# Performance work log

Measured on AMD Instinct MI355X. Metric: run time of the kernel, lower is better.

## Reference

```python
import jax, jax.numpy as jnp
import numpy as np

B, IN, H, CTX = 16384, 1024, 1024, 2048


def setup_inputs() -> dict:
    key = jax.random.key(0)
    ks = jax.random.split(key, 20)
    stdv = 1.0 / np.sqrt(H)
    u = lambda k, shape: jax.random.uniform(k, shape, jnp.float32, -stdv, stdv)
    inp = {
        "y": jax.random.normal(ks[0], (B, IN), jnp.float32),
        "ctx": jax.random.normal(ks[1], (B, CTX), jnp.float32),
        "c0": jax.random.normal(ks[2], (B, H), jnp.float32),
        "h0": jax.random.normal(ks[3], (B, H), jnp.float32),
        # Concatenated gate weights in order (i, f, o, c), matching the
        # per-gate matrices Wi..Wc, Ui..Uc, Ci..Cc of the original module.
        "W": u(ks[4], (4 * H, IN)),   # input projections
        "U": u(ks[5], (4 * H, H)),    # hidden projections
        "C": u(ks[6], (4 * H, CTX)),  # context projections
        "b": u(ks[7], (4 * H,)),      # gate biases
    }
    return inp


def reference(y, ctx, c0, h0, W, U, C, b):
    # One fused GEMM per input stream instead of 12 small ones; same math.
    gates = y @ W.T + h0 @ U.T + ctx @ C.T + b  # [B, 4H]
    gi, gf, go, gc = jnp.split(gates, 4, axis=-1)
    i = jax.nn.sigmoid(gi)
    f = jax.nn.sigmoid(gf)
    o = jax.nn.sigmoid(go)
    c_hat = jnp.tanh(gc)
    c = i * c_hat + f * c0
    h = o * jnp.tanh(c)
    return (c, h)
```

## Files before the change

### kernel.cpp

```cpp
#include <hip/hip_runtime.h>
#include <hip/hip_bf16.h>
#include <stdint.h>

typedef __attribute__((ext_vector_type(8))) short short8;
typedef __attribute__((ext_vector_type(8))) unsigned short ushort8;
typedef __attribute__((ext_vector_type(4))) float f32x4;
typedef __attribute__((ext_vector_type(8))) __bf16 bf16x8;

#define GAS __attribute__((address_space(1)))
#define LAS __attribute__((address_space(3)))

static constexpr int Bn = 16384;
static constexpr int Hn = 1024;
static constexpr int KT = 4096;
static constexpr int BM = 256;
static constexpr int NT = KT / 64;

#define SBAR()   __builtin_amdgcn_s_barrier()
#define VMCNT(n) asm volatile("s_waitcnt vmcnt(" #n ")" ::: "memory")

__device__ __forceinline__ unsigned short f2bf(float f) {
  unsigned u = __builtin_bit_cast(unsigned, f);
  u = (u + 0x7FFFu + ((u >> 16) & 1u)) >> 16;
  return (unsigned short)u;
}

__device__ __forceinline__ float fast_sigm(float x) {
  return __builtin_amdgcn_rcpf(1.f + __expf(-x));
}
__device__ __forceinline__ float fast_tanh(float x) {
  return 1.f - 2.f * __builtin_amdgcn_rcpf(__expf(2.f * x) + 1.f);
}

__global__ __launch_bounds__(256) void cvt_concat_k(
    const float* __restrict__ s0, const float* __restrict__ s1,
    const float* __restrict__ s2, unsigned short* __restrict__ dst,
    long long n8) {
  long long stride = (long long)gridDim.x * blockDim.x;
  for (long long g = (long long)blockIdx.x * blockDim.x + threadIdx.x; g < n8;
       g += stride) {
    long long row = g >> 9;
    int cg = (int)(g & 511) << 3;
    const float* src;
    if (cg < 1024)      src = s0 + row * 1024 + cg;
    else if (cg < 2048) src = s1 + row * 1024 + (cg - 1024);
    else                src = s2 + row * 2048 + (cg - 2048);
    float4 f0 = *(const float4*)src;
    float4 f1 = *(const float4*)(src + 4);
    ushort8 o;
    o[0] = f2bf(f0.x); o[1] = f2bf(f0.y); o[2] = f2bf(f0.z); o[3] = f2bf(f0.w);
    o[4] = f2bf(f1.x); o[5] = f2bf(f1.y); o[6] = f2bf(f1.z); o[7] = f2bf(f1.w);
    *(ushort8*)(dst + (g << 3)) = o;
  }
}

__global__ __launch_bounds__(512, 2) void lstm_gemm(
    const unsigned short* __restrict__ X, const unsigned short* __restrict__ Wc,
    const float* __restrict__ bias, const float* __restrict__ c0,
    float* __restrict__ out_c, float* __restrict__ out_h) {
  extern __shared__ char smem[];

  int bid = blockIdx.x;
  int swz = (bid & 7) * 128 + (bid >> 3);
  int mblk = swz >> 4, cblk = swz & 15;
  int brow0 = mblk * BM;
  int hcol0 = cblk * 64;

  int tid = threadIdx.x;
  int lane = tid & 63, wid = tid >> 6;
  int wr = wid >> 2, wc = wid & 3;

  const char* Xc = (const char*)X;
  const char* Wcc = (const char*)Wc;

  int rr = tid >> 3;
  uint32_t cbyte = (uint32_t)(((tid & 7) * 16) ^ ((rr & 7) << 4));
  uint32_t aoff[2][2], boff[2][2];
#pragma unroll
  for (int half = 0; half < 2; ++half) {
#pragma unroll
    for (int j = 0; j < 2; ++j) {
      int r = half * 128 + j * 64 + rr;
      aoff[half][j] = (uint32_t)(brow0 + r) * (KT * 2) + cbyte;
      int w = ((r >> 4) & 3) * 1024 + hcol0 + ((r >> 6) << 4) + (r & 15);
      boff[half][j] = (uint32_t)w * (KT * 2) + cbyte;
    }
  }

  auto stage_half = [&](int isB, int half, int tt) {
    int ts = tt < NT ? tt : NT - 1;
    int bufs = tt & 1;
#pragma unroll
    for (int j = 0; j < 2; ++j) {
      uint32_t off = (isB ? boff[half][j] : aoff[half][j]) + (uint32_t)ts * 128u;
      const char* src = (isB ? Wcc : Xc) + off;
      char* dst = smem + bufs * 65536 + isB * 32768 + half * 16384 + j * 8192 +
                  wid * 1024;
      __builtin_amdgcn_global_load_lds((const GAS unsigned int*)src,
                                       (LAS unsigned int*)dst, 16, 0, 0);
    }
  };

  int kg = (lane >> 4) << 4;
  int sw = (lane & 7) << 4;
  int koff0 = (0 + kg) ^ sw;
  int koff1 = (64 + kg) ^ sw;
  int fr = lane & 15;

  f32x4 acc[8][4] = {};
  short8 bfr[4][2];

  stage_half(1, 0, 0);
  stage_half(1, 1, 0);
  stage_half(0, 0, 0);
  stage_half(0, 1, 0);
  stage_half(1, 0, 1);
  stage_half(1, 1, 1);
  stage_half(0, 0, 1);
  VMCNT(8);
  SBAR();

  for (int t = 0; t < NT; ++t) {
    int p = t & 1;
#pragma unroll
    for (int q = 0; q < 4; ++q) {
      if (q == 0) {
        int bb = p * 65536 + 32768 + (wc * 64 + fr) * 128;
#pragma unroll
        for (int n = 0; n < 4; ++n) {
          bfr[n][0] = *(const short8*)(smem + bb + n * 2048 + koff0);
          bfr[n][1] = *(const short8*)(smem + bb + n * 2048 + koff1);
        }
      }
      int ab = p * 65536 + ((2 * q + wr) * 32 + fr) * 128;
      short8 a0k0 = *(const short8*)(smem + ab + koff0);
      short8 a0k1 = *(const short8*)(smem + ab + koff1);
      short8 a1k0 = *(const short8*)(smem + ab + 2048 + koff0);
      short8 a1k1 = *(const short8*)(smem + ab + 2048 + koff1);

      if (q == 0)      stage_half(0, 1, t + 1);
      else if (q == 1) stage_half(1, 0, t + 2);
      else if (q == 2) stage_half(1, 1, t + 2);
      else             stage_half(0, 0, t + 2);

      SBAR();
      __builtin_amdgcn_s_setprio(1);
#pragma unroll
      for (int n = 0; n < 4; ++n) {
        acc[2 * q][n] = __builtin_amdgcn_mfma_f32_16x16x32_bf16(
            __builtin_bit_cast(bf16x8, a0k0), __builtin_bit_cast(bf16x8, bfr[n][0]),
            acc[2 * q][n], 0, 0, 0);
        acc[2 * q][n] = __builtin_amdgcn_mfma_f32_16x16x32_bf16(
            __builtin_bit_cast(bf16x8, a0k1), __builtin_bit_cast(bf16x8, bfr[n][1]),
            acc[2 * q][n], 0, 0, 0);
        acc[2 * q + 1][n] = __builtin_amdgcn_mfma_f32_16x16x32_bf16(
            __builtin_bit_cast(bf16x8, a1k0), __builtin_bit_cast(bf16x8, bfr[n][0]),
            acc[2 * q + 1][n], 0, 0, 0);
        acc[2 * q + 1][n] = __builtin_amdgcn_mfma_f32_16x16x32_bf16(
            __builtin_bit_cast(bf16x8, a1k1), __builtin_bit_cast(bf16x8, bfr[n][1]),
            acc[2 * q + 1][n], 0, 0, 0);
      }
      __builtin_amdgcn_s_setprio(0);

      if (q == 1) { VMCNT(10); }
      else if (q == 3) { VMCNT(8); }
      SBAR();
    }
  }

  int col = hcol0 + wc * 16 + fr;
  float bi = bias[col], bf_ = bias[1024 + col];
  float bo = bias[2048 + col], bc = bias[3072 + col];
#pragma unroll
  for (int m = 0; m < 8; ++m) {
    int row0 = brow0 + (2 * (m >> 1) + wr) * 32 + (m & 1) * 16 + ((lane >> 4) << 2);
#pragma unroll
    for (int j = 0; j < 4; ++j) {
      size_t idx = (size_t)(row0 + j) * 1024 + col;
      float i_ = fast_sigm(acc[m][0][j] + bi);
      float f_ = fast_sigm(acc[m][1][j] + bf_);
      float o_ = fast_sigm(acc[m][2][j] + bo);
      float ch = fast_tanh(acc[m][3][j] + bc);
      float cn = i_ * ch + f_ * c0[idx];
      out_c[idx] = cn;
      out_h[idx] = o_ * fast_tanh(cn);
    }
  }
}

__global__ __launch_bounds__(256) void lstm_naive(
    const float* __restrict__ y, const float* __restrict__ ctx,
    const float* __restrict__ c0, const float* __restrict__ h0,
    const float* __restrict__ W, const float* __restrict__ U,
    const float* __restrict__ C, const float* __restrict__ b,
    float* __restrict__ out_c, float* __restrict__ out_h) {
  size_t t = (size_t)blockIdx.x * blockDim.x + threadIdx.x;
  if (t >= (size_t)Bn * Hn) return;
  int row = (int)(t >> 10), col = (int)(t & 1023);
  float g[4];
#pragma unroll
  for (int gg = 0; gg < 4; ++gg) {
    int wrow = gg * 1024 + col;
    float s = b[wrow];
    const float* yr = y + (size_t)row * 1024;
    const float* Wr = W + (size_t)wrow * 1024;
    for (int k = 0; k < 1024; ++k) s += yr[k] * Wr[k];
    const float* hr = h0 + (size_t)row * 1024;
    const float* Ur = U + (size_t)wrow * 1024;
    for (int k = 0; k < 1024; ++k) s += hr[k] * Ur[k];
    const float* cr = ctx + (size_t)row * 2048;
    const float* Cr = C + (size_t)wrow * 2048;
    for (int k = 0; k < 2048; ++k) s += cr[k] * Cr[k];
    g[gg] = s;
  }
  float i_ = fast_sigm(g[0]), f_ = fast_sigm(g[1]);
  float o_ = fast_sigm(g[2]), ch = fast_tanh(g[3]);
  float cn = i_ * ch + f_ * c0[t];
  out_c[t] = cn;
  out_h[t] = o_ * fast_tanh(cn);
}

extern "C" void kernel_launch(void* const* d_in, const int* in_sizes, int n_in,
                              void* d_out, int out_size, void* d_ws, size_t ws_size,
                              hipStream_t stream) {
  const float* y   = (const float*)d_in[0];
  const float* ctx = (const float*)d_in[1];
  const float* c0  = (const float*)d_in[2];
  const float* h0  = (const float*)d_in[3];
  const float* W   = (const float*)d_in[4];
  const float* U   = (const float*)d_in[5];
  const float* C   = (const float*)d_in[6];
  const float* b   = (const float*)d_in[7];
  float* out = (float*)d_out;
  float* out_c = out;
  float* out_h = out + (size_t)Bn * Hn;

  const size_t needX = (size_t)Bn * KT * 2;
  const size_t needW = (size_t)(4 * Hn) * KT * 2;

  if (ws_size >= needX + needW) {
    unsigned short* Xb = (unsigned short*)d_ws;
    unsigned short* Wb = (unsigned short*)((char*)d_ws + needX);
    cvt_concat_k<<<2048, 256, 0, stream>>>(y, h0, ctx, Xb, (long long)Bn * 512);
    cvt_concat_k<<<2048, 256, 0, stream>>>(W, U, C, Wb, (long long)(4 * Hn) * 512);
    (void)hipFuncSetAttribute((const void*)lstm_gemm,
                              hipFuncAttributeMaxDynamicSharedMemorySize, 131072);
    lstm_gemm<<<1024, 512, 131072, stream>>>(Xb, Wb, b, c0, out_c, out_h);
  } else {
    lstm_naive<<<(Bn * Hn + 255) / 256, 256, 0, stream>>>(y, ctx, c0, h0, W, U, C,
                                                          b, out_c, out_h);
  }
}
```

Measured before the change: 557.2 us.

## Load B fragments directly to registers and triple-buffer A tiles in LDS

The weight (B) operand is no longer staged through shared memory. Each wave loads its B fragments straight from global memory into registers, double-buffered across even and odd tiles. The A tile is now triple-buffered in LDS with a single barrier per K-tile instead of one per quarter-step. The block-to-tile swizzle is also changed so consecutive blocks share the same weight columns. The aims are to cut LDS traffic and barrier count and improve L2 reuse of the weights. The cost is more VGPR pressure and uncoalesced per-lane global loads for B.

```diff
diff --git a/kernel.cpp b/kernel.cpp
--- a/kernel.cpp
+++ b/kernel.cpp
@@ -13,11 +13,11 @@
 static constexpr int Bn = 16384;
 static constexpr int Hn = 1024;
 static constexpr int KT = 4096;
-static constexpr int BM = 256;
 static constexpr int NT = KT / 64;
 
 #define SBAR()   __builtin_amdgcn_s_barrier()
 #define VMCNT(n) asm volatile("s_waitcnt vmcnt(" #n ")" ::: "memory")
+#define FENCE()  asm volatile("" ::: "memory")
 
 __device__ __forceinline__ unsigned short f2bf(float f) {
   unsigned u = __builtin_bit_cast(unsigned, f);
@@ -62,8 +62,8 @@
 
   int bid = blockIdx.x;
   int swz = (bid & 7) * 128 + (bid >> 3);
-  int mblk = swz >> 4, cblk = swz & 15;
-  int brow0 = mblk * BM;
+  int mblk = swz & 63, cblk = swz >> 6;
+  int brow0 = mblk * 256;
   int hcol0 = cblk * 64;
 
   int tid = threadIdx.x;
@@ -75,27 +75,17 @@
 
   int rr = tid >> 3;
   uint32_t cbyte = (uint32_t)(((tid & 7) * 16) ^ ((rr & 7) << 4));
-  uint32_t aoff[2][2], boff[2][2];
-#pragma unroll
-  for (int half = 0; half < 2; ++half) {
-#pragma unroll
-    for (int j = 0; j < 2; ++j) {
-      int r = half * 128 + j * 64 + rr;
-      aoff[half][j] = (uint32_t)(brow0 + r) * (KT * 2) + cbyte;
-      int w = ((r >> 4) & 3) * 1024 + hcol0 + ((r >> 6) << 4) + (r & 15);
-      boff[half][j] = (uint32_t)w * (KT * 2) + cbyte;
-    }
-  }
-
-  auto stage_half = [&](int isB, int half, int tt) {
+  uint32_t aoffj[4];
+#pragma unroll
+  for (int j = 0; j < 4; ++j)
+    aoffj[j] = (uint32_t)(brow0 + j * 64 + rr) * (KT * 2) + cbyte;
+
+  auto stage_A = [&](int tt, int dbuf) {
     int ts = tt < NT ? tt : NT - 1;
-    int bufs = tt & 1;
-#pragma unroll
-    for (int j = 0; j < 2; ++j) {
-      uint32_t off = (isB ? boff[half][j] : aoff[half][j]) + (uint32_t)ts * 128u;
-      const char* src = (isB ? Wcc : Xc) + off;
-      char* dst = smem + bufs * 65536 + isB * 32768 + half * 16384 + j * 8192 +
-                  wid * 1024;
+#pragma unroll
+    for (int j = 0; j < 4; ++j) {
+      const char* src = Xc + aoffj[j] + (uint32_t)ts * 128u;
+      char* dst = smem + dbuf * 32768 + j * 8192 + wid * 1024;
       __builtin_amdgcn_global_load_lds((const GAS unsigned int*)src,
                                        (LAS unsigned int*)dst, 16, 0, 0);
     }
@@ -103,70 +93,82 @@
 
   int kg = (lane >> 4) << 4;
   int sw = (lane & 7) << 4;
-  int koff0 = (0 + kg) ^ sw;
+  int koff0 = kg ^ sw;
   int koff1 = (64 + kg) ^ sw;
   int fr = lane & 15;
 
+  const char* bbp[4];
+#pragma unroll
+  for (int n = 0; n < 4; ++n) {
+    int wrow = n * 1024 + hcol0 + wc * 16 + fr;
+    bbp[n] = Wcc + (size_t)wrow * (KT * 2) + ((lane >> 4) << 4);
+  }
+
   f32x4 acc[8][4] = {};
-  short8 bfr[4][2];
-
-  stage_half(1, 0, 0);
-  stage_half(1, 1, 0);
-  stage_half(0, 0, 0);
-  stage_half(0, 1, 0);
-  stage_half(1, 0, 1);
-  stage_half(1, 1, 1);
-  stage_half(0, 0, 1);
-  VMCNT(8);
-  SBAR();
-
-  for (int t = 0; t < NT; ++t) {
-    int p = t & 1;
-#pragma unroll
-    for (int q = 0; q < 4; ++q) {
-      if (q == 0) {
-        int bb = p * 65536 + 32768 + (wc * 64 + fr) * 128;
-#pragma unroll
-        for (int n = 0; n < 4; ++n) {
-          bfr[n][0] = *(const short8*)(smem + bb + n * 2048 + koff0);
-          bfr[n][1] = *(const short8*)(smem + bb + n * 2048 + koff1);
-        }
-      }
-      int ab = p * 65536 + ((2 * q + wr) * 32 + fr) * 128;
-      short8 a0k0 = *(const short8*)(smem + ab + koff0);
-      short8 a0k1 = *(const short8*)(smem + ab + koff1);
-      short8 a1k0 = *(const short8*)(smem + ab + 2048 + koff0);
-      short8 a1k1 = *(const short8*)(smem + ab + 2048 + koff1);
-
-      if (q == 0)      stage_half(0, 1, t + 1);
-      else if (q == 1) stage_half(1, 0, t + 2);
-      else if (q == 2) stage_half(1, 1, t + 2);
-      else             stage_half(0, 0, t + 2);
-
-      SBAR();
-      __builtin_amdgcn_s_setprio(1);
-#pragma unroll
-      for (int n = 0; n < 4; ++n) {
-        acc[2 * q][n] = __builtin_amdgcn_mfma_f32_16x16x32_bf16(
-            __builtin_bit_cast(bf16x8, a0k0), __builtin_bit_cast(bf16x8, bfr[n][0]),
-            acc[2 * q][n], 0, 0, 0);
-        acc[2 * q][n] = __builtin_amdgcn_mfma_f32_16x16x32_bf16(
-            __builtin_bit_cast(bf16x8, a0k1), __builtin_bit_cast(bf16x8, bfr[n][1]),
-            acc[2 * q][n], 0, 0, 0);
-        acc[2 * q + 1][n] = __builtin_amdgcn_mfma_f32_16x16x32_bf16(
-            __builtin_bit_cast(bf16x8, a1k0), __builtin_bit_cast(bf16x8, bfr[n][0]),
-            acc[2 * q + 1][n], 0, 0, 0);
-        acc[2 * q + 1][n] = __builtin_amdgcn_mfma_f32_16x16x32_bf16(
-            __builtin_bit_cast(bf16x8, a1k1), __builtin_bit_cast(bf16x8, bfr[n][1]),
-            acc[2 * q + 1][n], 0, 0, 0);
-      }
-      __builtin_amdgcn_s_setprio(0);
-
-      if (q == 1) { VMCNT(10); }
-      else if (q == 3) { VMCNT(8); }
-      SBAR();
-    }
-  }
+  short8 bfrE[4][2], bfrO[4][2];
+
+  stage_A(0, 0);
+  FENCE();
+#pragma unroll
+  for (int n = 0; n < 4; ++n) {
+    bfrE[n][0] = *(const short8*)(bbp[n]);
+    bfrE[n][1] = *(const short8*)(bbp[n] + 64);
+  }
+  stage_A(1, 1);
+
+  int bufA = 0;
+
+#define TILE(T_, BC, BN)                                                      \
+  {                                                                           \
+    VMCNT(12);                                                                \
+    SBAR();                                                                   \
+    int pb = bufA * 32768;                                                    \
+    int stg = bufA + 2; if (stg >= 3) stg -= 3;                               \
+    _Pragma("unroll")                                                         \
+    for (int q = 0; q < 4; ++q) {                                             \
+      int ab = pb + ((2 * q + wr) * 32 + fr) * 128;                           \
+      short8 a0 = *(const short8*)(smem + ab + koff0);                        \
+      short8 a1 = *(const short8*)(smem + ab + koff1);                        \
+      short8 a2 = *(const short8*)(smem + ab + 2048 + koff0);                 \
+      short8 a3 = *(const short8*)(smem + ab + 2048 + koff1);                 \
+      if (q == 1) {                \
+        int ts = (T_) + 1 < NT ? (T_) + 1 : NT - 1;                           \
+        _Pragma("unroll")                                                     \
+        for (int n = 0; n < 4; ++n) {                                         \
+          BN[n][0] = *(const short8*)(bbp[n] + (size_t)ts * 128);             \
+          BN[n][1] = *(const short8*)(bbp[n] + (size_t)ts * 128 + 64);        \
+        }                                                                     \
+      }                                                                       \
+      if (q == 3) stage_A((T_) + 2, stg);                                     \
+      __builtin_amdgcn_s_setprio(1);                                          \
+      _Pragma("unroll")                                                       \
+      for (int n = 0; n < 4; ++n) {                                           \
+        acc[2 * q][n] = __builtin_amdgcn_mfma_f32_16x16x32_bf16(              \
+            __builtin_bit_cast(bf16x8, a0), __builtin_bit_cast(bf16x8, BC[n][0]),\
+            acc[2 * q][n], 0, 0, 0);                                          \
+        acc[2 * q + 1][n] = __builtin_amdgcn_mfma_f32_16x16x32_bf16(          \
+            __builtin_bit_cast(bf16x8, a2), __builtin_bit_cast(bf16x8, BC[n][0]),\
+            acc[2 * q + 1][n], 0, 0, 0);                                      \
+      }                                                                       \
+      _Pragma("unroll")                                                       \
+      for (int n = 0; n < 4; ++n) {                                           \
+        acc[2 * q][n] = __builtin_amdgcn_mfma_f32_16x16x32_bf16(              \
+            __builtin_bit_cast(bf16x8, a1), __builtin_bit_cast(bf16x8, BC[n][1]),\
+            acc[2 * q][n], 0, 0, 0);                                          \
+        acc[2 * q + 1][n] = __builtin_amdgcn_mfma_f32_16x16x32_bf16(          \
+            __builtin_bit_cast(bf16x8, a3), __builtin_bit_cast(bf16x8, BC[n][1]),\
+            acc[2 * q + 1][n], 0, 0, 0);                                      \
+      }                                                                       \
+      __builtin_amdgcn_s_setprio(0);                                          \
+    }                                                                         \
+    bufA = bufA + 1; if (bufA >= 3) bufA = 0;                                 \
+  }
+
+  for (int t = 0; t < NT; t += 2) {
+    TILE(t, bfrE, bfrO)
+    TILE(t + 1, bfrO, bfrE)
+  }
+#undef TILE
 
   int col = hcol0 + wc * 16 + fr;
   float bi = bias[col], bf_ = bias[1024 + col];
@@ -244,8 +246,8 @@
     cvt_concat_k<<<2048, 256, 0, stream>>>(y, h0, ctx, Xb, (long long)Bn * 512);
     cvt_concat_k<<<2048, 256, 0, stream>>>(W, U, C, Wb, (long long)(4 * Hn) * 512);
     (void)hipFuncSetAttribute((const void*)lstm_gemm,
-                              hipFuncAttributeMaxDynamicSharedMemorySize, 131072);
-    lstm_gemm<<<1024, 512, 131072, stream>>>(Xb, Wb, b, c0, out_c, out_h);
+                              hipFuncAttributeMaxDynamicSharedMemorySize, 98304);
+    lstm_gemm<<<1024, 512, 98304, stream>>>(Xb, Wb, b, c0, out_c, out_h);
   } else {
     lstm_naive<<<(Bn * Hn + 255) / 256, 256, 0, stream>>>(y, ctx, c0, h0, W, U, C,
                                                           b, out_c, out_h);
```

Measured after the change: 694.6 us. +24.7%, slower.
